# Performance work log

Measured on AMD Instinct MI355X. Metric: run time of the kernel, lower is better.

Reference implementation:

```python
import jax, jax.numpy as jnp
import numpy as np

STEP = 1.0  # module init arg
N = 8192


def setup_inputs() -> dict:
    key = jax.random.key(0)
    k1, = jax.random.split(key, 1)
    predictions = jax.random.normal(k1, (N, 1), dtype=jnp.float32) * 50.0  # depth-like values
    z_spacing = jnp.ones((), dtype=jnp.float32) * 2.5
    nth_slice = jnp.ones((), dtype=jnp.float32) * 4.0
    return {"predictions": predictions, "z_spacing": z_spacing, "nth_slice": nth_slice}


def reference(predictions, z_spacing, nth_slice):
    p = predictions[:, 0]                       # [N]
    n = p.shape[0]
    acceptable_step = STEP * z_spacing * nth_slice
    # closed form of the loop-built step matrix: steps[i,j] = |i-j| * acceptable_step
    idx = jnp.arange(n)
    steps = jnp.abs(idx[:, None] - idx[None, :]).astype(p.dtype) * acceptable_step  # [N,N]
    d = p[:, None] - p[None, :]                 # [N,N] pairwise differences
    # first masked update: where d >= 0, subtract 0.2*steps
    d = jnp.where(d >= 0, d - 0.2 * steps, d)
    # second masked update on the updated d: clamp (d - 0.8*steps) at 0
    d = jnp.where(d >= 0, jnp.maximum(d - 0.8 * steps, jnp.zeros((), d.dtype)), d)
    loss = jnp.sum(jnp.abs(jnp.tril(d))) / (n * n)
    return loss
```

## Files before the change

kernel.cpp:

```cpp
#include <hip/hip_runtime.h>


typedef float f32x2 __attribute__((ext_vector_type(2)));

constexpr int ROWS = 256;
constexpr int COLS = 64;

__global__ __launch_bounds__(ROWS) void depth_loss_kernel(
    const float* __restrict__ p,
    const float* __restrict__ zsp,
    const float* __restrict__ nsl,
    double* __restrict__ partials)
{
    int b = blockIdx.x;
    int ri = (int)((sqrtf(2.0f * (float)b + 1.0f) - 1.0f) * 0.5f);
    while (2 * (ri + 1) * (ri + 2) <= b) ++ri;
    while (2 * ri * (ri + 1) > b) --ri;
    int cj = b - 2 * ri * (ri + 1);

    int tid = threadIdx.x;
    int i = ri * ROWS + tid;
    float pi = p[i];

    __shared__ __align__(16) float pj[COLS];
    int jbase = cj * COLS;
    if (tid < COLS / 4)
        ((float4*)pj)[tid] = ((const float4*)(p + jbase))[tid];
    __syncthreads();

    float a   = zsp[0] * nsl[0];
    float a02 = 0.2f * a;
    f32x2 av   = { a,   a   };
    f32x2 a02v = { a02, a02 };
    f32x2 four = { 4.0f, 4.0f };
    f32x2 zero = { 0.0f, 0.0f };
    f32x2 pi2  = { pi, pi };

    float dij0 = (float)(i - jbase);
    f32x2 d2a = { dij0,        dij0 - 1.0f };
    f32x2 d2b = { dij0 - 2.0f, dij0 - 3.0f };

    f32x2 acc2a = zero, acc2b = zero;
    const float4* pj4 = (const float4*)pj;

#define GROUP_BODY(VA, D2, ACC, MASKED)                               \
    {                                                                 \
        f32x2 n0 = (VA) - pi2;                         \
        f32x2 e1 = __builtin_elementwise_fma(D2, a02v, n0);           \
        f32x2 t  = __builtin_elementwise_fma(D2, av,   n0);           \
        f32x2 cp = __builtin_elementwise_max(                         \
                       __builtin_elementwise_max(e1, -t), zero);      \
        f32x2 c;                                                      \
        c.x = (n0.x > 0.0f) ? n0.x : cp.x;                            \
        c.y = (n0.y > 0.0f) ? n0.y : cp.y;                            \
        if (MASKED) {                                                 \
            c.x = (D2.x >= 0.0f) ? c.x : 0.0f;                        \
            c.y = (D2.y >= 0.0f) ? c.y : 0.0f;                        \
        }                                                             \
        ACC += c;                                       \
        D2  -= four;                                    \
    }

    if (cj < 4 * ri) {
        #pragma unroll
        for (int q = 0; q < COLS / 4; ++q) {
            float4 v = pj4[q];
            f32x2 va = { v.x, v.y };
            f32x2 vb = { v.z, v.w };
            GROUP_BODY(va, d2a, acc2a, false)
            GROUP_BODY(vb, d2b, acc2b, false)
        }
    } else {
        #pragma unroll
        for (int q = 0; q < COLS / 4; ++q) {
            float4 v = pj4[q];
            f32x2 va = { v.x, v.y };
            f32x2 vb = { v.z, v.w };
            GROUP_BODY(va, d2a, acc2a, true)
            GROUP_BODY(vb, d2b, acc2b, true)
        }
    }
#undef GROUP_BODY

    float acc = (acc2a.x + acc2a.y) + (acc2b.x + acc2b.y);

    for (int off = 32; off > 0; off >>= 1)
        acc += __shfl_down(acc, off, 64);

    __shared__ float wsum[ROWS / 64];
    if ((tid & 63) == 0) wsum[tid >> 6] = acc;
    __syncthreads();

    if (tid == 0) {
        float blocksum = 0.0f;
        for (int w = 0; w < ROWS / 64; ++w) blocksum += wsum[w];
        partials[blockIdx.x] = (double)blocksum;
    }
}

__global__ __launch_bounds__(256) void finalize_kernel(
    const double* __restrict__ partials, int nblocks, float* __restrict__ out,
    double inv_nn)
{
    int tid = threadIdx.x;
    double acc = 0.0;
    for (int b = tid; b < nblocks; b += 256) acc += partials[b];
    for (int off = 32; off > 0; off >>= 1)
        acc += __shfl_down(acc, off, 64);
    __shared__ double wsum[4];
    if ((tid & 63) == 0) wsum[tid >> 6] = acc;
    __syncthreads();
    if (tid == 0)
        out[0] = (float)((wsum[0] + wsum[1] + wsum[2] + wsum[3]) * inv_nn);
}

extern "C" void kernel_launch(void* const* d_in, const int* in_sizes, int n_in,
                              void* d_out, int out_size, void* d_ws, size_t ws_size,
                              hipStream_t stream) {
    const float* p   = (const float*)d_in[0];
    const float* zsp = (const float*)d_in[1];
    const float* nsl = (const float*)d_in[2];
    float* out = (float*)d_out;
    double* partials = (double*)d_ws;

    int n = in_sizes[0];
    int nrt = (n + ROWS - 1) / ROWS;
    int nblocks = 2 * nrt * (nrt + 1);
    double inv_nn = 1.0 / ((double)n * (double)n);

    depth_loss_kernel<<<nblocks, ROWS, 0, stream>>>(p, zsp, nsl, partials);
    finalize_kernel<<<1, 256, 0, stream>>>(partials, nblocks, out, inv_nn);
}
```

Measured before the change: 67.61 us.

## Fuse reduction into persistent cooperative kernel with grid sync and wider tiles

Replaces the one-block-per-tile launch (about 2112 tiny blocks of 256x64) with a persistent grid of 1024 blocks that loop over 256x128 tiles. The final reduction now runs inside the same kernel after a cooperative grid sync, removing the second kernel launch. If the cooperative launch fails, it falls back to a non-cooperative kernel plus the old finalize kernel. The aims are to cut launch and per-block setup overhead. The cost is grid-sync latency and a less even tile distribution across blocks.

```diff
diff --git a/kernel.cpp b/kernel.cpp
--- a/kernel.cpp
+++ b/kernel.cpp
@@ -1,86 +1,87 @@
 #include <hip/hip_runtime.h>
+#include <hip/hip_cooperative_groups.h>
+
+namespace cg = cooperative_groups;
 
 
 typedef float f32x2 __attribute__((ext_vector_type(2)));
 
 constexpr int ROWS = 256;
-constexpr int COLS = 64;
+constexpr int COLS = 128;
+constexpr int GRID = 1024;
 
-__global__ __launch_bounds__(ROWS) void depth_loss_kernel(
-    const float* __restrict__ p,
-    const float* __restrict__ zsp,
-    const float* __restrict__ nsl,
-    double* __restrict__ partials)
+__device__ __forceinline__ float block_tiles_sum(
+    const float* __restrict__ p, float a, int ntiles, int tid, float* pjs)
 {
-    int b = blockIdx.x;
-    int ri = (int)((sqrtf(2.0f * (float)b + 1.0f) - 1.0f) * 0.5f);
-    while (2 * (ri + 1) * (ri + 2) <= b) ++ri;
-    while (2 * ri * (ri + 1) > b) --ri;
-    int cj = b - 2 * ri * (ri + 1);
-
-    int tid = threadIdx.x;
-    int i = ri * ROWS + tid;
-    float pi = p[i];
-
-    __shared__ __align__(16) float pj[COLS];
-    int jbase = cj * COLS;
-    if (tid < COLS / 4)
-        ((float4*)pj)[tid] = ((const float4*)(p + jbase))[tid];
-    __syncthreads();
-
-    float a   = zsp[0] * nsl[0];
     float a02 = 0.2f * a;
     f32x2 av   = { a,   a   };
     f32x2 a02v = { a02, a02 };
     f32x2 four = { 4.0f, 4.0f };
     f32x2 zero = { 0.0f, 0.0f };
-    f32x2 pi2  = { pi, pi };
-
-    float dij0 = (float)(i - jbase);
-    f32x2 d2a = { dij0,        dij0 - 1.0f };
-    f32x2 d2b = { dij0 - 2.0f, dij0 - 3.0f };
 
     f32x2 acc2a = zero, acc2b = zero;
-    const float4* pj4 = (const float4*)pj;
+
+    for (int b = blockIdx.x; b < ntiles; b += GRID) {
+        int ri = (int)((sqrtf(4.0f * (float)b + 1.0f) - 1.0f) * 0.5f);
+        while ((ri + 1) * (ri + 2) <= b) ++ri;
+        while (ri * (ri + 1) > b) --ri;
+        int cj = b - ri * (ri + 1);
+
+        int i = ri * ROWS + tid;
+        float pi = p[i];
+        f32x2 pi2 = { pi, pi };
+
+        int jbase = cj * COLS;
+        if (tid < COLS / 4)
+            ((float4*)pjs)[tid] = ((const float4*)(p + jbase))[tid];
+        __syncthreads();
+
+        float dij0 = (float)(i - jbase);
+        f32x2 d2a = { dij0,        dij0 - 1.0f };
+        f32x2 d2b = { dij0 - 2.0f, dij0 - 3.0f };
+
+        const float4* pj4 = (const float4*)pjs;
 
 #define GROUP_BODY(VA, D2, ACC, MASKED)                               \
-    {                                                                 \
-        f32x2 n0 = (VA) - pi2;                         \
-        f32x2 e1 = __builtin_elementwise_fma(D2, a02v, n0);           \
-        f32x2 t  = __builtin_elementwise_fma(D2, av,   n0);           \
-        f32x2 cp = __builtin_elementwise_max(                         \
-                       __builtin_elementwise_max(e1, -t), zero);      \
-        f32x2 c;                                                      \
-        c.x = (n0.x > 0.0f) ? n0.x : cp.x;                            \
-        c.y = (n0.y > 0.0f) ? n0.y : cp.y;                            \
-        if (MASKED) {                                                 \
-            c.x = (D2.x >= 0.0f) ? c.x : 0.0f;                        \
-            c.y = (D2.y >= 0.0f) ? c.y : 0.0f;                        \
-        }                                                             \
-        ACC += c;                                       \
-        D2  -= four;                                    \
+        {                                                             \
+            f32x2 n0 = (VA) - pi2;                      \
+            f32x2 e1 = __builtin_elementwise_fma(D2, a02v, n0);       \
+            f32x2 t  = __builtin_elementwise_fma(D2, av,   n0);       \
+            f32x2 cp = __builtin_elementwise_max(                     \
+                           __builtin_elementwise_max(e1, -t), zero);  \
+            f32x2 c;                                                  \
+            c.x = (n0.x > 0.0f) ? n0.x : cp.x;                        \
+            c.y = (n0.y > 0.0f) ? n0.y : cp.y;                        \
+            if (MASKED) {                                             \
+                c.x = (D2.x >= 0.0f) ? c.x : 0.0f;                    \
+                c.y = (D2.y >= 0.0f) ? c.y : 0.0f;                    \
+            }                                                         \
+            ACC += c;                                   \
+            D2  -= four;                                \
+        }
+
+        if (cj < 2 * ri) {
+            #pragma unroll 8
+            for (int q = 0; q < COLS / 4; ++q) {
+                float4 v = pj4[q];
+                f32x2 va = { v.x, v.y };
+                f32x2 vb = { v.z, v.w };
+                GROUP_BODY(va, d2a, acc2a, false)
+                GROUP_BODY(vb, d2b, acc2b, false)
+            }
+        } else {
+            #pragma unroll 8
+            for (int q = 0; q < COLS / 4; ++q) {
+                float4 v = pj4[q];
+                f32x2 va = { v.x, v.y };
+                f32x2 vb = { v.z, v.w };
+                GROUP_BODY(va, d2a, acc2a, true)
+                GROUP_BODY(vb, d2b, acc2b, true)
+            }
+        }
+#undef GROUP_BODY
+        __syncthreads();
     }
-
-    if (cj < 4 * ri) {
-        #pragma unroll
-        for (int q = 0; q < COLS / 4; ++q) {
-            float4 v = pj4[q];
-            f32x2 va = { v.x, v.y };
-            f32x2 vb = { v.z, v.w };
-            GROUP_BODY(va, d2a, acc2a, false)
-            GROUP_BODY(vb, d2b, acc2b, false)
-        }
-    } else {
-        #pragma unroll
-        for (int q = 0; q < COLS / 4; ++q) {
-            float4 v = pj4[q];
-            f32x2 va = { v.x, v.y };
-            f32x2 vb = { v.z, v.w };
-            GROUP_BODY(va, d2a, acc2a, true)
-            GROUP_BODY(vb, d2b, acc2b, true)
-        }
-    }
-#undef GROUP_BODY
 
     float acc = (acc2a.x + acc2a.y) + (acc2b.x + acc2b.y);
 
@@ -91,11 +92,62 @@
     if ((tid & 63) == 0) wsum[tid >> 6] = acc;
     __syncthreads();
 
-    if (tid == 0) {
-        float blocksum = 0.0f;
-        for (int w = 0; w < ROWS / 64; ++w) blocksum += wsum[w];
-        partials[blockIdx.x] = (double)blocksum;
+    float bs = 0.0f;
+    if (tid == 0)
+        bs = (wsum[0] + wsum[1]) + (wsum[2] + wsum[3]);
+    return bs;
+}
+
+__global__ __launch_bounds__(ROWS, 4) void depth_loss_coop(
+    const float* __restrict__ p,
+    const float* __restrict__ zsp,
+    const float* __restrict__ nsl,
+    double* __restrict__ partials,
+    float* __restrict__ out,
+    int n)
+{
+    __shared__ __align__(16) float pjs[COLS];
+    int tid = threadIdx.x;
+    int nrt = n / ROWS;
+    int ntiles = nrt * (nrt + 1);
+    float a = zsp[0] * nsl[0];
+
+    float bs = block_tiles_sum(p, a, ntiles, tid, pjs);
+    if (tid == 0) partials[blockIdx.x] = (double)bs;
+    __threadfence();
+    cg::this_grid().sync();
+
+    if (blockIdx.x == 0) {
+        double acc = partials[tid]       + partials[tid + 256]
+                   + partials[tid + 512] + partials[tid + 768];
+        for (int off = 32; off > 0; off >>= 1)
+            acc += __shfl_down(acc, off, 64);
+        __shared__ double wsumd[ROWS / 64];
+        if ((tid & 63) == 0) wsumd[tid >> 6] = acc;
+        __syncthreads();
+        if (tid == 0) {
+            double inv_nn = 1.0 / ((double)n * (double)n);
+            out[0] = (float)(((wsumd[0] + wsumd[1]) + (wsumd[2] + wsumd[3])) * inv_nn);
+        }
     }
+}
+
+
+__global__ __launch_bounds__(ROWS, 4) void depth_loss_nosync(
+    const float* __restrict__ p,
+    const float* __restrict__ zsp,
+    const float* __restrict__ nsl,
+    double* __restrict__ partials,
+    int n)
+{
+    __shared__ __align__(16) float pjs[COLS];
+    int tid = threadIdx.x;
+    int nrt = n / ROWS;
+    int ntiles = nrt * (nrt + 1);
+    float a = zsp[0] * nsl[0];
+
+    float bs = block_tiles_sum(p, a, ntiles, tid, pjs);
+    if (tid == 0) partials[blockIdx.x] = (double)bs;
 }
 
 __global__ __launch_bounds__(256) void finalize_kernel(
@@ -111,7 +163,7 @@
     if ((tid & 63) == 0) wsum[tid >> 6] = acc;
     __syncthreads();
     if (tid == 0)
-        out[0] = (float)((wsum[0] + wsum[1] + wsum[2] + wsum[3]) * inv_nn);
+        out[0] = (float)(((wsum[0] + wsum[1]) + (wsum[2] + wsum[3])) * inv_nn);
 }
 
 extern "C" void kernel_launch(void* const* d_in, const int* in_sizes, int n_in,
@@ -124,10 +176,15 @@
     double* partials = (double*)d_ws;
 
     int n = in_sizes[0];
-    int nrt = (n + ROWS - 1) / ROWS;
-    int nblocks = 2 * nrt * (nrt + 1);
-    double inv_nn = 1.0 / ((double)n * (double)n);
 
-    depth_loss_kernel<<<nblocks, ROWS, 0, stream>>>(p, zsp, nsl, partials);
-    finalize_kernel<<<1, 256, 0, stream>>>(partials, nblocks, out, inv_nn);
+    void* args[] = { (void*)&p, (void*)&zsp, (void*)&nsl,
+                     (void*)&partials, (void*)&out, (void*)&n };
+    hipError_t err = hipLaunchCooperativeKernel(
+        (const void*)depth_loss_coop, dim3(GRID), dim3(ROWS), args, 0, stream);
+
+    if (err != hipSuccess) {
+        double inv_nn = 1.0 / ((double)n * (double)n);
+        depth_loss_nosync<<<GRID, ROWS, 0, stream>>>(p, zsp, nsl, partials, n);
+        finalize_kernel<<<1, 256, 0, stream>>>(partials, GRID, out, inv_nn);
+    }
 }
```

New measurement: 180.8 us. 2.67x slower.

## Enlarge tiles to two rows per thread and fuse finalize via atomics

Applied to the files above, without the earlier changes.

Each thread now handles two rows against a 128-column shared tile, which reuses every loaded column value twice and cuts the grid to about a quarter as many blocks. The separate finalize kernel is replaced by a double-precision atomicAdd plus a completion counter, and the last block writes the output. The workspace header is zeroed with a memset each launch. In exchange it adds atomics and a memset launch, and the row-tile count now assumes n is divisible by 512.

```diff
diff --git a/kernel.cpp b/kernel.cpp
--- a/kernel.cpp
+++ b/kernel.cpp
@@ -3,14 +3,19 @@
 
 typedef float f32x2 __attribute__((ext_vector_type(2)));
 
-constexpr int ROWS = 256;
-constexpr int COLS = 64;
+constexpr int TPB  = 256;
+constexpr int TR   = 512;
+constexpr int COLS = 128;
 
-__global__ __launch_bounds__(ROWS) void depth_loss_kernel(
+struct WsHeader { double acc; unsigned int cnt; unsigned int pad; };
+
+__global__ __launch_bounds__(TPB, 3) void depth_loss_fused(
     const float* __restrict__ p,
     const float* __restrict__ zsp,
     const float* __restrict__ nsl,
-    double* __restrict__ partials)
+    WsHeader* __restrict__ hdr,
+    float* __restrict__ out,
+    int n, int nblocks)
 {
     int b = blockIdx.x;
     int ri = (int)((sqrtf(2.0f * (float)b + 1.0f) - 1.0f) * 0.5f);
@@ -19,13 +24,17 @@
     int cj = b - 2 * ri * (ri + 1);
 
     int tid = threadIdx.x;
-    int i = ri * ROWS + tid;
-    float pi = p[i];
+    int i0 = ri * TR + tid;
+    int i1 = i0 + TPB;
+    float pi0 = p[i0];
+    float pi1 = p[i1];
+    f32x2 pi2_0 = { pi0, pi0 };
+    f32x2 pi2_1 = { pi1, pi1 };
 
-    __shared__ __align__(16) float pj[COLS];
+    __shared__ __align__(16) float pjs[COLS];
     int jbase = cj * COLS;
     if (tid < COLS / 4)
-        ((float4*)pj)[tid] = ((const float4*)(p + jbase))[tid];
+        ((float4*)pjs)[tid] = ((const float4*)(p + jbase))[tid];
     __syncthreads();
 
     float a   = zsp[0] * nsl[0];
@@ -34,18 +43,19 @@
     f32x2 a02v = { a02, a02 };
     f32x2 four = { 4.0f, 4.0f };
     f32x2 zero = { 0.0f, 0.0f };
-    f32x2 pi2  = { pi, pi };
 
-    float dij0 = (float)(i - jbase);
-    f32x2 d2a = { dij0,        dij0 - 1.0f };
-    f32x2 d2b = { dij0 - 2.0f, dij0 - 3.0f };
+    float dij0 = (float)(i0 - jbase);
+    f32x2 d2a0 = { dij0,          dij0 - 1.0f };
+    f32x2 d2b0 = { dij0 - 2.0f,   dij0 - 3.0f };
+    f32x2 d2a1 = { dij0 + 256.0f, dij0 + 255.0f };
+    f32x2 d2b1 = { dij0 + 254.0f, dij0 + 253.0f };
 
-    f32x2 acc2a = zero, acc2b = zero;
-    const float4* pj4 = (const float4*)pj;
+    f32x2 acc2a0 = zero, acc2b0 = zero, acc2a1 = zero, acc2b1 = zero;
+    const float4* pj4 = (const float4*)pjs;
 
-#define GROUP_BODY(VA, D2, ACC, MASKED)                               \
+#define GROUP_BODY(VA, PI2, D2, ACC, MASKED)                          \
     {                                                                 \
-        f32x2 n0 = (VA) - pi2;                         \
+        f32x2 n0 = (VA) - PI2;                         \
         f32x2 e1 = __builtin_elementwise_fma(D2, a02v, n0);           \
         f32x2 t  = __builtin_elementwise_fma(D2, av,   n0);           \
         f32x2 cp = __builtin_elementwise_max(                         \
@@ -62,56 +72,52 @@
     }
 
     if (cj < 4 * ri) {
-        #pragma unroll
+        #pragma unroll 4
         for (int q = 0; q < COLS / 4; ++q) {
             float4 v = pj4[q];
             f32x2 va = { v.x, v.y };
             f32x2 vb = { v.z, v.w };
-            GROUP_BODY(va, d2a, acc2a, false)
-            GROUP_BODY(vb, d2b, acc2b, false)
+            GROUP_BODY(va, pi2_0, d2a0, acc2a0, false)
+            GROUP_BODY(vb, pi2_0, d2b0, acc2b0, false)
+            GROUP_BODY(va, pi2_1, d2a1, acc2a1, false)
+            GROUP_BODY(vb, pi2_1, d2b1, acc2b1, false)
         }
     } else {
-        #pragma unroll
+        #pragma unroll 4
         for (int q = 0; q < COLS / 4; ++q) {
             float4 v = pj4[q];
             f32x2 va = { v.x, v.y };
             f32x2 vb = { v.z, v.w };
-            GROUP_BODY(va, d2a, acc2a, true)
-            GROUP_BODY(vb, d2b, acc2b, true)
+            GROUP_BODY(va, pi2_0, d2a0, acc2a0, true)
+            GROUP_BODY(vb, pi2_0, d2b0, acc2b0, true)
+            GROUP_BODY(va, pi2_1, d2a1, acc2a1, true)
+            GROUP_BODY(vb, pi2_1, d2b1, acc2b1, true)
         }
     }
 #undef GROUP_BODY
 
-    float acc = (acc2a.x + acc2a.y) + (acc2b.x + acc2b.y);
+    f32x2 acc2 = (acc2a0 + acc2b0) + (acc2a1 + acc2b1);
+    float acc = acc2.x + acc2.y;
 
     for (int off = 32; off > 0; off >>= 1)
         acc += __shfl_down(acc, off, 64);
 
-    __shared__ float wsum[ROWS / 64];
+    __shared__ float wsum[TPB / 64];
     if ((tid & 63) == 0) wsum[tid >> 6] = acc;
     __syncthreads();
 
     if (tid == 0) {
-        float blocksum = 0.0f;
-        for (int w = 0; w < ROWS / 64; ++w) blocksum += wsum[w];
-        partials[blockIdx.x] = (double)blocksum;
+        double bs = (double)((wsum[0] + wsum[1]) + (wsum[2] + wsum[3]));
+        atomicAdd(&hdr->acc, bs);
+        __threadfence();
+        unsigned int old = atomicAdd(&hdr->cnt, 1u);
+        if (old == (unsigned int)(nblocks - 1)) {
+            __threadfence();
+            double tot = atomicAdd(&hdr->acc, 0.0);
+            double inv_nn = 1.0 / ((double)n * (double)n);
+            out[0] = (float)(tot * inv_nn);
+        }
     }
-}
-
-__global__ __launch_bounds__(256) void finalize_kernel(
-    const double* __restrict__ partials, int nblocks, float* __restrict__ out,
-    double inv_nn)
-{
-    int tid = threadIdx.x;
-    double acc = 0.0;
-    for (int b = tid; b < nblocks; b += 256) acc += partials[b];
-    for (int off = 32; off > 0; off >>= 1)
-        acc += __shfl_down(acc, off, 64);
-    __shared__ double wsum[4];
-    if ((tid & 63) == 0) wsum[tid >> 6] = acc;
-    __syncthreads();
-    if (tid == 0)
-        out[0] = (float)((wsum[0] + wsum[1] + wsum[2] + wsum[3]) * inv_nn);
 }
 
 extern "C" void kernel_launch(void* const* d_in, const int* in_sizes, int n_in,
@@ -121,13 +127,12 @@
     const float* zsp = (const float*)d_in[1];
     const float* nsl = (const float*)d_in[2];
     float* out = (float*)d_out;
-    double* partials = (double*)d_ws;
+    WsHeader* hdr = (WsHeader*)d_ws;
 
     int n = in_sizes[0];
-    int nrt = (n + ROWS - 1) / ROWS;
+    int nrt = n / TR;
     int nblocks = 2 * nrt * (nrt + 1);
-    double inv_nn = 1.0 / ((double)n * (double)n);
 
-    depth_loss_kernel<<<nblocks, ROWS, 0, stream>>>(p, zsp, nsl, partials);
-    finalize_kernel<<<1, 256, 0, stream>>>(partials, nblocks, out, inv_nn);
+    hipMemsetAsync(d_ws, 0, sizeof(WsHeader), stream);
+    depth_loss_fused<<<nblocks, TPB, 0, stream>>>(p, zsp, nsl, hdr, out, n, nblocks);
 }
```

Result: slower. 75.70 us (+12.0%).
